# Performance work log

Measured on AMD Instinct MI355X. Metric: run time of the kernel, lower is better.

Reference implementation:

```python
import jax, jax.numpy as jnp
import numpy as np

N_BLOCKS = 2
C = 64
N_HEADS = 4
FF = 256
NB_SEQ = 40
SEQ_LEN = 512
NB_PAIRS = (NB_SEQ * (NB_SEQ - 1)) // 2  # 780
B = 2
EPS_ATT = 1e-6


def _ln(x, g, b, eps=1e-5):
    # LayerNorm over last axis (channels)
    mu = jnp.mean(x, axis=-1, keepdims=True)
    var = jnp.var(x, axis=-1, keepdims=True)
    return (x - mu) * jax.lax.rsqrt(var + eps) * g + b


def _kernel_attn(x, wq, bq, wk, bk, wv, bv, wp, bp):
    # x: [B, M, T, C]; faithful to KernelAxialMultiAttention.
    Bs, M, T, Cc = x.shape
    N, D = N_HEADS, Cc // N_HEADS
    q = jax.nn.elu(x @ wq.T + bq) + 1.0
    k = jax.nn.elu(x @ wk.T + bk) + 1.0
    v = x @ wv.T + bv
    q = q.reshape(Bs, M, T, N, D)
    k = k.reshape(Bs, M, T, N, D)
    v = v.reshape(Bs, M, T, N, D)
    ksum = k.sum(axis=2)                                   # [B,M,N,D]
    z = 1.0 / (jnp.einsum('bmtnd,bmnd->bmtn', q, ksum) + EPS_ATT)  # [B,M,T,N]
    ktv = jnp.einsum('bmtnd,bmtne->bmnde', k, v)           # [B,M,N,D,D]
    # Original does Z.expand(...,T,D) @ KtV where Z's D columns are identical,
    # which equals z * column-sum of KtV (sum over first D axis).
    ktv_cs = ktv.sum(axis=-2)                              # [B,M,N,D]
    V = z[..., None] * ktv_cs[:, :, None, :, :]            # [B,M,T,N,D]
    V = V.reshape(Bs, M, T, Cc)
    return V @ wp.T + bp


def setup_inputs() -> dict:
    key = jax.random.key(0)
    ks = iter(jax.random.split(key, 64))

    def w(shape, scale=0.05):
        return jax.random.normal(next(ks), shape, dtype=jnp.float32) * scale

    # seq2pair gather matrix [P, S]
    ii, jj = np.triu_indices(NB_SEQ, 1)
    sp = np.zeros((NB_PAIRS, NB_SEQ), np.float32)
    sp[np.arange(NB_PAIRS), ii] = 1.0
    sp[np.arange(NB_PAIRS), jj] = 1.0

    inp = {
        'x': jax.random.normal(next(ks), (B, 22, SEQ_LEN, NB_SEQ), dtype=jnp.float32),
        'w_in': w((C, 22)), 'b_in': jnp.zeros((C,), jnp.float32),
        'g0': jnp.ones((C,), jnp.float32), 'be0': jnp.zeros((C,), jnp.float32),
        'rqw': w((N_BLOCKS, C, C)), 'rqb': jnp.zeros((N_BLOCKS, C), jnp.float32),
        'rkw': w((N_BLOCKS, C, C)), 'rkb': jnp.zeros((N_BLOCKS, C), jnp.float32),
        'rvw': w((N_BLOCKS, C, C)), 'rvb': jnp.zeros((N_BLOCKS, C), jnp.float32),
        'rpw': w((N_BLOCKS, C, C)), 'rpb': jnp.zeros((N_BLOCKS, C), jnp.float32),
        'cqw': w((N_BLOCKS, C, C)), 'cqb': jnp.zeros((N_BLOCKS, C), jnp.float32),
        'ckw': w((N_BLOCKS, C, C)), 'ckb': jnp.zeros((N_BLOCKS, C), jnp.float32),
        'cvw': w((N_BLOCKS, C, C)), 'cvb': jnp.zeros((N_BLOCKS, C), jnp.float32),
        'cpw': w((N_BLOCKS, C, C)), 'cpb': jnp.zeros((N_BLOCKS, C), jnp.float32),
        'ln_g': jnp.ones((N_BLOCKS, C), jnp.float32), 'ln_b': jnp.zeros((N_BLOCKS, C), jnp.float32),
        'f1w': w((N_BLOCKS, FF, C)), 'f1b': jnp.zeros((N_BLOCKS, FF), jnp.float32),
        'f2w': w((N_BLOCKS, C, FF)), 'f2b': jnp.zeros((N_BLOCKS, C), jnp.float32),
        'wout': w((1, C)), 'bout': jnp.zeros((1,), jnp.float32),
        'seq2pair': jnp.asarray(sp),
    }
    return inp


def reference(x, w_in, b_in, g0, be0, rqw, rqb, rkw, rkb, rvw, rvb, rpw, rpb,
              cqw, cqb, ckw, ckb, cvw, cvb, cpw, cpb, ln_g, ln_b,
              f1w, f1b, f2w, f2b, wout, bout, seq2pair):
    # block_1_1: 1x1 conv (22->64) + ReLU; x: [B,22,L,S] -> h: [B,C,L,S]
    h = jax.nn.relu(jnp.einsum('bcls,dc->bdls', x, w_in) + b_in[None, :, None, None])
    # seq2pair gather-sum: [B,P,L,C] channel-last representation
    hp = jnp.einsum('ps,bdls->bpld', seq2pair, h)
    hp = _ln(hp, g0, be0)
    for i in range(N_BLOCKS):
        # row attention over seq_len axis (M=P, T=L)
        att = _kernel_attn(hp, rqw[i], rqb[i], rkw[i], rkb[i], rvw[i], rvb[i], rpw[i], rpb[i])
        hp = att + hp
        hp = _ln(hp, ln_g[i], ln_b[i])
        # column attention over pairs axis (M=L, T=P)
        hc = jnp.swapaxes(hp, 1, 2)  # [B,L,P,C]
        att = _kernel_attn(hc, cqw[i], cqb[i], ckw[i], ckb[i], cvw[i], cvb[i], cpw[i], cpb[i])
        hp = jnp.swapaxes(att, 1, 2) + hp
        hp = _ln(hp, ln_g[i], ln_b[i])
        # FFN: 1x1 conv 64->256 GELU 256->64, residual
        f = jax.nn.gelu(hp @ f1w[i].T + f1b[i], approximate=False)
        hp = (f @ f2w[i].T + f2b[i]) + hp
        if i != N_BLOCKS - 1:
            hp = _ln(hp, ln_g[i], ln_b[i])
    # pwFNN: 1x1 conv 64->1 + Softplus, then mean over seq_len axis
    y = jax.nn.softplus(hp @ wout.T + bout)[..., 0]   # [B,P,L]
    return jnp.mean(y, axis=-1)                        # [B,P]
```

## Files before the change

kernel.cpp:

```cpp
#include <hip/hip_runtime.h>
#include <math.h>
#include <stdint.h>

#define B_   2
#define S_   40
#define P_   780
#define L_   512
#define C_   64
#define FF_  256
#define NTOK (B_*P_*L_)

typedef __attribute__((ext_vector_type(8))) short short8;
typedef __attribute__((ext_vector_type(4))) float f32x4;
typedef __attribute__((ext_vector_type(4))) unsigned short us4;

__device__ __forceinline__ float ln64(float r, float g, float b) {
    float s1 = r, s2 = r * r;
    #pragma unroll
    for (int m = 1; m < 64; m <<= 1) {
        s1 += __shfl_xor(s1, m, 64);
        s2 += __shfl_xor(s2, m, 64);
    }
    float mu  = s1 * (1.0f / 64.0f);
    float var = s2 * (1.0f / 64.0f) - mu * mu;
    return (r - mu) * rsqrtf(var + 1e-5f) * g + b;
}
__device__ __forceinline__ float gelu_fast(float x) {
    float x2 = x * x;
    float u  = x * fmaf(0.044715f, x2, 1.0f);
    float e  = __builtin_amdgcn_exp2f(u * 2.302265106f);
    return x * e * __builtin_amdgcn_rcpf(e + 1.0f);
}
__device__ __forceinline__ float softplus_f(float v) {
    return (v > 20.0f) ? v : log1pf(__expf(v));
}
__device__ __forceinline__ float elup1(float v) {
    return (v > 0.0f) ? v + 1.0f : __expf(v);
}
__device__ __forceinline__ unsigned short f2bf(float f) {
    union { float f; uint32_t u; } cv; cv.f = f;
    uint32_t u = cv.u;
    return (unsigned short)((u + 0x7FFFu + ((u >> 16) & 1u)) >> 16);
}
__device__ __forceinline__ float bf2f(unsigned short u) {
    union { uint32_t u; float f; } cv; cv.u = (uint32_t)u << 16; return cv.f;
}
__device__ __forceinline__ float bflo(uint32_t w) {
    union { uint32_t u; float f; } cv; cv.u = w << 16; return cv.f;
}
__device__ __forceinline__ float bfhi(uint32_t w) {
    union { uint32_t u; float f; } cv; cv.u = w & 0xffff0000u; return cv.f;
}
__device__ __forceinline__ uint32_t cvtpk(float a, float b) {
    uint32_t d;
    asm("v_cvt_pk_bf16_f32 %0, %1, %2" : "=v"(d) : "v"(a), "v"(b));
    return d;
}

__global__ void k_conv_in(const float* __restrict__ x, const float* __restrict__ w_in,
                          const float* __restrict__ b_in, float* __restrict__ h) {
    int gid = blockIdx.x * 256 + threadIdx.x;
    int c  = gid & 63;
    int tk = gid >> 6;
    if (tk >= B_ * L_ * S_) return;
    int b = tk / (L_ * S_);
    int r = tk % (L_ * S_);
    int l = r / S_;
    int s = r % S_;
    float acc = b_in[c];
    const float* xb = x + (size_t)b * 22 * L_ * S_ + (size_t)l * S_ + s;
    #pragma unroll
    for (int cc = 0; cc < 22; cc++)
        acc = fmaf(xb[(size_t)cc * L_ * S_], w_in[c * 22 + cc], acc);
    h[gid] = fmaxf(acc, 0.0f);
}

__global__ void k_gather_ln(const float* __restrict__ h, const float* __restrict__ g0,
                            const float* __restrict__ be0, unsigned short* __restrict__ hp) {
    int lane = threadIdx.x & 63;
    int wv   = threadIdx.x >> 6;
    int tk = blockIdx.x * 4 + wv;
    if (tk >= NTOK) return;
    int b = tk / (P_ * L_);
    int r = tk % (P_ * L_);
    int p = r / L_;
    int l = r % L_;
    int i = 0, rem = p, cnt = S_ - 1;
    while (rem >= cnt) { rem -= cnt; cnt--; i++; }
    int j = i + 1 + rem;
    const float* hb = h + (((size_t)b * L_ + l) * S_) * 64;
    float v = hb[i * 64 + lane] + hb[j * 64 + lane];
    hp[(size_t)tk * 64 + lane] = f2bf(ln64(v, g0[lane], be0[lane]));
}

__global__ void k_wprep_qkv(const float* __restrict__ rqw, const float* __restrict__ rkw,
                            const float* __restrict__ rvw, const float* __restrict__ cqw,
                            const float* __restrict__ ckw, const float* __restrict__ cvw,
                            unsigned short* __restrict__ qkvf) {
    int g = blockIdx.x * 256 + threadIdx.x;
    if (g >= 6144) return;
    int m = g >> 9, r = g & 511;
    int mat = m >> 1, layer = m & 1;
    int q = r >> 6, lane = r & 63;
    int c = lane & 15, hi = lane >> 4;
    int nt = q >> 1, s = q & 1;
    const float* base;
    switch (mat) {
        case 0: base = rqw; break; case 1: base = rkw; break; case 2: base = rvw; break;
        case 3: base = cqw; break; case 4: base = ckw; break; default: base = cvw; break;
    }
    const float* src = base + layer * 4096 + (nt * 16 + c) * 64 + s * 32 + hi * 8;
    short8 v;
    #pragma unroll
    for (int i = 0; i < 8; i++) v[i] = (short)f2bf(src[i]);
    *(short8*)(qkvf + (size_t)m * 4096 + (size_t)r * 8) = v;
}

__global__ void k_wprep(const float* __restrict__ f1w, const float* __restrict__ f2w,
                        unsigned short* __restrict__ w1s, unsigned short* __restrict__ w2s) {
    int g = blockIdx.x * 256 + threadIdx.x;
    if (g >= 8192) return;
    int layer = g >> 12;
    int rem   = g & 4095;
    int which = rem >> 11;
    int idx   = rem & 2047;
    int l  = idx & 63;
    int q  = idx >> 6;
    int c  = l & 15, hi = l >> 4;
    const float* src;
    unsigned short* dst;
    if (which == 0) {
        int s = q & 1, nt = q >> 1;
        src = f1w + (size_t)layer * 16384 + (nt * 16 + c) * 64 + s * 32 + hi * 8;
        dst = w1s + (size_t)layer * 16384 + (size_t)idx * 8;
    } else {
        int s = q & 7, nt = q >> 3;
        src = f2w + (size_t)layer * 16384 + (nt * 16 + c) * 256 + s * 32 + hi * 8;
        dst = w2s + (size_t)layer * 16384 + (size_t)idx * 8;
    }
    short8 v;
    #pragma unroll
    for (int i = 0; i < 8; i++) v[i] = (short)f2bf(src[i]);
    *(short8*)dst = v;
}

__global__ __launch_bounds__(512) void k_row_fused(
        const unsigned short* __restrict__ hp, unsigned short* __restrict__ hpT,
        const unsigned short* __restrict__ wqf, const unsigned short* __restrict__ wkf,
        const unsigned short* __restrict__ wvf,
        const float* __restrict__ bq, const float* __restrict__ bk,
        const float* __restrict__ bv, const float* __restrict__ wp,
        const float* __restrict__ bp, const float* __restrict__ lng,
        const float* __restrict__ lnb) {
    __shared__ float redK[8][64];
    __shared__ float redV[8][64];
    __shared__ float kvfin[64];
    __shared__ float sksum[64];
    __shared__ float swkv[256];

    const int tid = threadIdx.x, lane = tid & 63, w8 = tid >> 6;
    const int t = lane & 15, hi = lane >> 4;
    const int slice = blockIdx.x;
    const size_t base = (size_t)slice * L_ * 64;

    short8 xkeep[4][2];
    float ks[4][4] = {}, kv[4][4] = {};
    {
        short8 wkfr[4][2], wvfr[4][2];
        #pragma unroll
        for (int nt = 0; nt < 4; nt++)
            #pragma unroll
            for (int s = 0; s < 2; s++) {
                wkfr[nt][s] = *(const short8*)(wkf + ((size_t)((nt*2+s)*64 + lane)) * 8);
                wvfr[nt][s] = *(const short8*)(wvf + ((size_t)((nt*2+s)*64 + lane)) * 8);
            }
        f32x4 bkL[4], bvL[4];
        #pragma unroll
        for (int nt = 0; nt < 4; nt++) {
            bkL[nt] = *(const f32x4*)(bk + nt * 16 + hi * 4);
            bvL[nt] = *(const f32x4*)(bv + nt * 16 + hi * 4);
        }
        #pragma unroll
        for (int it = 0; it < 4; it++) {
            int tok = (w8 + it * 8) * 16 + t;
            const unsigned short* src = hp + base + (size_t)tok * 64;
            #pragma unroll
            for (int s = 0; s < 2; s++)
                xkeep[it][s] = *(const short8*)(src + s * 32 + hi * 8);
            f32x4 aK[4], aV[4];
            #pragma unroll
            for (int nt = 0; nt < 4; nt++) { aK[nt] = (f32x4){0,0,0,0}; aV[nt] = (f32x4){0,0,0,0}; }
            #pragma unroll
            for (int nt = 0; nt < 4; nt++)
                #pragma unroll
                for (int s = 0; s < 2; s++) {
                    aK[nt] = __builtin_amdgcn_mfma_f32_16x16x32_bf16(wkfr[nt][s], xkeep[it][s], aK[nt], 0, 0, 0);
                    aV[nt] = __builtin_amdgcn_mfma_f32_16x16x32_bf16(wvfr[nt][s], xkeep[it][s], aV[nt], 0, 0, 0);
                }
            #pragma unroll
            for (int nt = 0; nt < 4; nt++) {
                float kk[4], vv[4];
                #pragma unroll
                for (int r = 0; r < 4; r++) {
                    kk[r] = elup1(aK[nt][r] + bkL[nt][r]);
                    vv[r] = aV[nt][r] + bvL[nt][r];
                }
                float sp = kk[0] + kk[1] + kk[2] + kk[3];
                sp += __shfl_xor(sp, 16, 64);
                sp += __shfl_xor(sp, 32, 64);
                #pragma unroll
                for (int r = 0; r < 4; r++) { ks[nt][r] += kk[r]; kv[nt][r] += sp * vv[r]; }
            }
        }
    }
    #pragma unroll
    for (int nt = 0; nt < 4; nt++)
        #pragma unroll
        for (int r = 0; r < 4; r++) {
            #pragma unroll
            for (int m = 1; m < 16; m <<= 1) {
                ks[nt][r] += __shfl_xor(ks[nt][r], m, 64);
                kv[nt][r] += __shfl_xor(kv[nt][r], m, 64);
            }
        }
    if (t == 0) {
        #pragma unroll
        for (int nt = 0; nt < 4; nt++)
            #pragma unroll
            for (int r = 0; r < 4; r++) {
                redK[w8][nt * 16 + hi * 4 + r] = ks[nt][r];
                redV[w8][nt * 16 + hi * 4 + r] = kv[nt][r];
            }
    }
    __syncthreads();
    if (tid < 64) {
        float a = 0.0f, b2 = 0.0f;
        #pragma unroll
        for (int w = 0; w < 8; w++) { a += redK[w][tid]; b2 += redV[w][tid]; }
        sksum[tid] = a;
        kvfin[tid] = b2;
    }
    __syncthreads();
    if (tid < 256) {
        int c = tid & 63, n = tid >> 6;
        const float* wpr = wp + c * 64 + n * 16;
        float s = 0.0f;
        #pragma unroll
        for (int e = 0; e < 16; e++) s = fmaf(kvfin[n * 16 + e], wpr[e], s);
        swkv[c * 4 + n] = s;
    }
    __syncthreads();

    short8 wqfr[4][2];
    #pragma unroll
    for (int nt = 0; nt < 4; nt++)
        #pragma unroll
        for (int s = 0; s < 2; s++)
            wqfr[nt][s] = *(const short8*)(wqf + ((size_t)((nt*2+s)*64 + lane)) * 8);
    f32x4 bqL[4], bpL[4], gL[4], bL[4];
    #pragma unroll
    for (int nt = 0; nt < 4; nt++) {
        bqL[nt] = *(const f32x4*)(bq + nt * 16 + hi * 4);
        bpL[nt] = *(const f32x4*)(bp + nt * 16 + hi * 4);
        gL[nt]  = *(const f32x4*)(lng + nt * 16 + hi * 4);
        bL[nt]  = *(const f32x4*)(lnb + nt * 16 + hi * 4);
    }
    const int bb = slice / P_, pp = slice - bb * P_;

    #pragma unroll
    for (int it = 0; it < 4; it++) {
        int tok = (w8 + it * 8) * 16 + t;
        f32x4 aQ[4];
        #pragma unroll
        for (int nt = 0; nt < 4; nt++) aQ[nt] = (f32x4){0,0,0,0};
        #pragma unroll
        for (int nt = 0; nt < 4; nt++)
            #pragma unroll
            for (int s = 0; s < 2; s++)
                aQ[nt] = __builtin_amdgcn_mfma_f32_16x16x32_bf16(wqfr[nt][s], xkeep[it][s], aQ[nt], 0, 0, 0);
        float z[4];
        #pragma unroll
        for (int nt = 0; nt < 4; nt++) {
            f32x4 kS = *(const f32x4*)(sksum + nt * 16 + hi * 4);
            float d = 0.0f;
            #pragma unroll
            for (int r = 0; r < 4; r++)
                d = fmaf(elup1(aQ[nt][r] + bqL[nt][r]), kS[r], d);
            d += __shfl_xor(d, 16, 64);
            d += __shfl_xor(d, 32, 64);
            z[nt] = 1.0f / (d + 1e-6f);
        }
        const unsigned short* srcr = hp + base + (size_t)tok * 64;
        float o[4][4];
        float s1 = 0.0f, s2 = 0.0f;
        #pragma unroll
        for (int nt = 0; nt < 4; nt++) {
            us4 xr4 = *(const us4*)(srcr + nt * 16 + hi * 4);
            #pragma unroll
            for (int r = 0; r < 4; r++) {
                int ch = nt * 16 + hi * 4 + r;
                f32x4 wv4 = *(const f32x4*)(swkv + ch * 4);
                float val = z[0] * wv4[0] + z[1] * wv4[1] + z[2] * wv4[2] + z[3] * wv4[3]
                          + bpL[nt][r] + bf2f(xr4[r]);
                o[nt][r] = val;
                s1 += val; s2 += val * val;
            }
        }
        s1 += __shfl_xor(s1, 16, 64);  s1 += __shfl_xor(s1, 32, 64);
        s2 += __shfl_xor(s2, 16, 64);  s2 += __shfl_xor(s2, 32, 64);
        float mu  = s1 * (1.0f / 64.0f);
        float var = s2 * (1.0f / 64.0f) - mu * mu;
        float rs  = rsqrtf(var + 1e-5f);
        unsigned short* dst = hpT + (((size_t)bb * L_ + tok) * P_ + pp) * 64;
        #pragma unroll
        for (int nt = 0; nt < 4; nt++) {
            float r0 = (o[nt][0] - mu) * rs * gL[nt][0] + bL[nt][0];
            float r1 = (o[nt][1] - mu) * rs * gL[nt][1] + bL[nt][1];
            float r2 = (o[nt][2] - mu) * rs * gL[nt][2] + bL[nt][2];
            float r3 = (o[nt][3] - mu) * rs * gL[nt][3] + bL[nt][3];
            *(uint2*)(dst + nt * 16 + hi * 4) = make_uint2(cvtpk(r0, r1), cvtpk(r2, r3));
        }
    }
}

__global__ __launch_bounds__(512) void k_col_red(
        const unsigned short* __restrict__ xb, const unsigned short* __restrict__ wkf,
        const unsigned short* __restrict__ wvf, const float* __restrict__ bk,
        const float* __restrict__ bv, const float* __restrict__ wp,
        float* __restrict__ stats) {
    __shared__ float redK[8][64];
    __shared__ float redV[8][64];
    __shared__ float kvfin[64];

    const int tid = threadIdx.x, lane = tid & 63, w8 = tid >> 6;
    const int t = lane & 15, hi = lane >> 4;
    const int slice = blockIdx.x;
    const size_t base = (size_t)slice * P_ * 64;

    short8 wkfr[4][2], wvfr[4][2];
    #pragma unroll
    for (int nt = 0; nt < 4; nt++)
        #pragma unroll
        for (int s = 0; s < 2; s++) {
            wkfr[nt][s] = *(const short8*)(wkf + ((size_t)((nt*2+s)*64 + lane)) * 8);
            wvfr[nt][s] = *(const short8*)(wvf + ((size_t)((nt*2+s)*64 + lane)) * 8);
        }
    f32x4 bkL[4], bvL[4];
    #pragma unroll
    for (int nt = 0; nt < 4; nt++) {
        bkL[nt] = *(const f32x4*)(bk + nt * 16 + hi * 4);
        bvL[nt] = *(const f32x4*)(bv + nt * 16 + hi * 4);
    }

    float ks[4][4] = {}, kv[4][4] = {};
    #pragma unroll 1
    for (int tile = w8; tile < 49; tile += 8) {
        int tok = tile * 16 + t;
        bool valid = tok < P_;
        int tokc = valid ? tok : (P_ - 1);
        const unsigned short* src = xb + base + (size_t)tokc * 64;
        short8 xf[2];
        #pragma unroll
        for (int s = 0; s < 2; s++)
            xf[s] = *(const short8*)(src + s * 32 + hi * 8);
        f32x4 aK[4], aV[4];
        #pragma unroll
        for (int nt = 0; nt < 4; nt++) { aK[nt] = (f32x4){0,0,0,0}; aV[nt] = (f32x4){0,0,0,0}; }
        #pragma unroll
        for (int nt = 0; nt < 4; nt++)
            #pragma unroll
            for (int s = 0; s < 2; s++) {
                aK[nt] = __builtin_amdgcn_mfma_f32_16x16x32_bf16(wkfr[nt][s], xf[s], aK[nt], 0, 0, 0);
                aV[nt] = __builtin_amdgcn_mfma_f32_16x16x32_bf16(wvfr[nt][s], xf[s], aV[nt], 0, 0, 0);
            }
        #pragma unroll
        for (int nt = 0; nt < 4; nt++) {
            float kk[4], vv[4];
            #pragma unroll
            for (int r = 0; r < 4; r++) {
                kk[r] = valid ? elup1(aK[nt][r] + bkL[nt][r]) : 0.0f;
                vv[r] = valid ? (aV[nt][r] + bvL[nt][r]) : 0.0f;
            }
            float sp = kk[0] + kk[1] + kk[2] + kk[3];
            sp += __shfl_xor(sp, 16, 64);
            sp += __shfl_xor(sp, 32, 64);
            #pragma unroll
            for (int r = 0; r < 4; r++) { ks[nt][r] += kk[r]; kv[nt][r] += sp * vv[r]; }
        }
    }

    #pragma unroll
    for (int nt = 0; nt < 4; nt++)
        #pragma unroll
        for (int r = 0; r < 4; r++) {
            #pragma unroll
            for (int m = 1; m < 16; m <<= 1) {
                ks[nt][r] += __shfl_xor(ks[nt][r], m, 64);
                kv[nt][r] += __shfl_xor(kv[nt][r], m, 64);
            }
        }
    if (t == 0) {
        #pragma unroll
        for (int nt = 0; nt < 4; nt++)
            #pragma unroll
            for (int r = 0; r < 4; r++) {
                redK[w8][nt * 16 + hi * 4 + r] = ks[nt][r];
                redV[w8][nt * 16 + hi * 4 + r] = kv[nt][r];
            }
    }
    __syncthreads();
    if (tid < 64) {
        float a = 0.0f, b2 = 0.0f;
        #pragma unroll
        for (int w = 0; w < 8; w++) { a += redK[w][tid]; b2 += redV[w][tid]; }
        stats[(size_t)slice * 320 + tid] = a;
        kvfin[tid] = b2;
    }
    __syncthreads();
    if (tid < 256) {
        int c = tid & 63, n = tid >> 6;
        const float* wpr = wp + c * 64 + n * 16;
        float s = 0.0f;
        #pragma unroll
        for (int e = 0; e < 16; e++) s = fmaf(kvfin[n * 16 + e], wpr[e], s);
        stats[(size_t)slice * 320 + 64 + c * 4 + n] = s;
    }
}

template <int MODE>
__global__ __launch_bounds__(256, 2) void k_cmap_ffn3(
        const unsigned short* __restrict__ hpT, unsigned short* __restrict__ hp,
        const unsigned short* __restrict__ wqf,
        const float* __restrict__ bq, const float* __restrict__ bpv,
        const float* __restrict__ stats,
        const unsigned short* __restrict__ w1s, const float* __restrict__ f1b,
        const unsigned short* __restrict__ w2s, const float* __restrict__ f2b,
        const float* __restrict__ lng, const float* __restrict__ lnb,
        const float* __restrict__ wout, const float* __restrict__ bout,
        float* __restrict__ out) {
    __shared__ __align__(16) unsigned char G2[4][3][4096];
    __shared__ float sstat[320];

    const int tid = threadIdx.x, lane = tid & 63, wv = tid >> 6;
    const int t = lane & 15, hi = lane >> 4;
    const int slice = blockIdx.x / 5, tb = blockIdx.x % 5;
    const int bb = slice >> 9, ll = slice & 511;
    const size_t base = (size_t)slice * P_ * 64;

    for (int i = tid; i < 320; i += 256) sstat[i] = stats[(size_t)slice * 320 + i];
    __syncthreads();
    if (tb * 12 + wv >= 49) return;

    short8 wqfr[4][2];
    #pragma unroll
    for (int nt = 0; nt < 4; nt++)
        #pragma unroll
        for (int s = 0; s < 2; s++)
            wqfr[nt][s] = *(const short8*)(wqf + ((size_t)((nt*2+s)*64 + lane)) * 8);
    f32x4 bqL[4], bpL[4], gL[4], bL[4], f2bL[4];
    #pragma unroll
    for (int nt = 0; nt < 4; nt++) {
        bqL[nt]  = *(const f32x4*)(bq  + nt * 16 + hi * 4);
        bpL[nt]  = *(const f32x4*)(bpv + nt * 16 + hi * 4);
        gL[nt]   = *(const f32x4*)(lng + nt * 16 + hi * 4);
        bL[nt]   = *(const f32x4*)(lnb + nt * 16 + hi * 4);
        f2bL[nt] = *(const f32x4*)(f2b + nt * 16 + hi * 4);
    }

    uint32_t pw[3][8];
    short8 xb2A[3][2];
    bool validA[3];
    int pcA[3];

    #pragma unroll
    for (int tt = 0; tt < 3; tt++) {
        int slot = tb * 12 + tt * 4 + wv;
        int slotc = (slot < 49) ? slot : 48;
        int p = slotc * 16 + t;
        bool valid = (slot < 49) && (p < P_);
        int pc = (p < P_) ? p : P_ - 1;
        validA[tt] = valid; pcA[tt] = pc;
        const unsigned short* src = hpT + base + (size_t)pc * 64;

        short8 xf[2];
        #pragma unroll
        for (int s = 0; s < 2; s++)
            xf[s] = *(const short8*)(src + s * 32 + hi * 8);
        f32x4 aQ[4];
        #pragma unroll
        for (int nt = 0; nt < 4; nt++) aQ[nt] = (f32x4){0,0,0,0};
        #pragma unroll
        for (int nt = 0; nt < 4; nt++)
            #pragma unroll
            for (int s = 0; s < 2; s++)
                aQ[nt] = __builtin_amdgcn_mfma_f32_16x16x32_bf16(wqfr[nt][s], xf[s], aQ[nt], 0, 0, 0);
        float z[4];
        #pragma unroll
        for (int nt = 0; nt < 4; nt++) {
            f32x4 kS = *(const f32x4*)(sstat + nt * 16 + hi * 4);
            float d = 0.0f;
            #pragma unroll
            for (int r = 0; r < 4; r++)
                d = fmaf(elup1(aQ[nt][r] + bqL[nt][r]), kS[r], d);
            d += __shfl_xor(d, 16, 64);
            d += __shfl_xor(d, 32, 64);
            z[nt] = 1.0f / (d + 1e-6f);
        }
        float vv[4][4];
        float s1 = 0.0f, s2 = 0.0f;
        #pragma unroll
        for (int nt = 0; nt < 4; nt++) {
            us4 xr4 = *(const us4*)(src + nt * 16 + hi * 4);
            #pragma unroll
            for (int r = 0; r < 4; r++) {
                int ch = nt * 16 + hi * 4 + r;
                f32x4 wv4 = *(const f32x4*)(sstat + 64 + ch * 4);
                float val = z[0] * wv4[0] + z[1] * wv4[1] + z[2] * wv4[2] + z[3] * wv4[3]
                          + bpL[nt][r] + bf2f(xr4[r]);
                vv[nt][r] = val;
                s1 += val; s2 += val * val;
            }
        }
        s1 += __shfl_xor(s1, 16, 64);  s1 += __shfl_xor(s1, 32, 64);
        s2 += __shfl_xor(s2, 16, 64);  s2 += __shfl_xor(s2, 32, 64);
        float mu  = s1 * (1.0f / 64.0f);
        float var = s2 * (1.0f / 64.0f) - mu * mu;
        float rs  = rsqrtf(var + 1e-5f);
        #pragma unroll
        for (int nt = 0; nt < 4; nt++) {
            float r0 = (vv[nt][0] - mu) * rs * gL[nt][0] + bL[nt][0];
            float r1 = (vv[nt][1] - mu) * rs * gL[nt][1] + bL[nt][1];
            float r2 = (vv[nt][2] - mu) * rs * gL[nt][2] + bL[nt][2];
            float r3 = (vv[nt][3] - mu) * rs * gL[nt][3] + bL[nt][3];
            pw[tt][nt * 2]     = cvtpk(r0, r1);
            pw[tt][nt * 2 + 1] = cvtpk(r2, r3);
        }

        unsigned char* yw = &G2[wv][tt][0];
        #pragma unroll
        for (int nt = 0; nt < 4; nt++) {
            uint32_t ch0 = nt * 16 + hi * 4;
            uint32_t boff = (uint32_t)t * 128 + ((ch0 >> 3) ^ (uint32_t)(t & 7)) * 16 + (ch0 & 7) * 2;
            *(uint2*)(yw + boff) = make_uint2(pw[tt][nt * 2], pw[tt][nt * 2 + 1]);
        }
        #pragma unroll
        for (int s = 0; s < 2; s++)
            xb2A[tt][s] = *(short8*)(yw + (uint32_t)t * 128 +
                                     (((uint32_t)(s * 4 + hi)) ^ (uint32_t)(t & 7)) * 16);
    }

    f32x4 acc2A[3][4];
    #pragma unroll
    for (int tt = 0; tt < 3; tt++)
        #pragma unroll
        for (int n2 = 0; n2 < 4; n2++) acc2A[tt][n2] = f2bL[n2];

    #pragma unroll
    for (int half = 0; half < 2; half++) {
        #pragma unroll
        for (int ntl = 0; ntl < 8; ntl++) {
            int nt = half * 8 + ntl;
            f32x4 b1 = *(const f32x4*)(f1b + nt * 16 + hi * 4);
            f32x4 accA[3] = { b1, b1, b1 };
            #pragma unroll
            for (int s = 0; s < 2; s++) {
                short8 wf = *(const short8*)(w1s + ((size_t)(nt * 2 + s) * 64 + lane) * 8);
                accA[0] = __builtin_amdgcn_mfma_f32_16x16x32_bf16(wf, xb2A[0][s], accA[0], 0, 0, 0);
                accA[1] = __builtin_amdgcn_mfma_f32_16x16x32_bf16(wf, xb2A[1][s], accA[1], 0, 0, 0);
                accA[2] = __builtin_amdgcn_mfma_f32_16x16x32_bf16(wf, xb2A[2][s], accA[2], 0, 0, 0);
            }
            uint32_t woff = ((uint32_t)(ntl * 32 + hi * 8)) ^ ((uint32_t)(t & 7) << 4);
            #pragma unroll
            for (int tt = 0; tt < 3; tt++) {
                uint32_t p0 = cvtpk(gelu_fast(accA[tt][0]), gelu_fast(accA[tt][1]));
                uint32_t p1 = cvtpk(gelu_fast(accA[tt][2]), gelu_fast(accA[tt][3]));
                *(uint2*)(&G2[wv][tt][0] + t * 256 + woff) = make_uint2(p0, p1);
            }
        }
        #pragma unroll
        for (int sl = 0; sl < 4; sl++) {
            int s = half * 4 + sl;
            uint32_t roff = ((uint32_t)(sl * 64 + hi * 16)) ^ ((uint32_t)(t & 7) << 4);
            short8 faA[3];
            #pragma unroll
            for (int tt = 0; tt < 3; tt++)
                faA[tt] = *(short8*)(&G2[wv][tt][0] + t * 256 + roff);
            #pragma unroll
            for (int n2 = 0; n2 < 4; n2++) {
                short8 wf = *(const short8*)(w2s + ((size_t)(n2 * 8 + s) * 64 + lane) * 8);
                acc2A[0][n2] = __builtin_amdgcn_mfma_f32_16x16x32_bf16(wf, faA[0], acc2A[0][n2], 0, 0, 0);
                acc2A[1][n2] = __builtin_amdgcn_mfma_f32_16x16x32_bf16(wf, faA[1], acc2A[1][n2], 0, 0, 0);
                acc2A[2][n2] = __builtin_amdgcn_mfma_f32_16x16x32_bf16(wf, faA[2], acc2A[2][n2], 0, 0, 0);
            }
        }
    }

    #pragma unroll
    for (int tt = 0; tt < 3; tt++) {
        float vo[4][4];
        float s1 = 0.0f, s2 = 0.0f;
        #pragma unroll
        for (int n2 = 0; n2 < 4; n2++) {
            float y0 = bflo(pw[tt][n2 * 2]);
            float y1 = bfhi(pw[tt][n2 * 2]);
            float y2 = bflo(pw[tt][n2 * 2 + 1]);
            float y3 = bfhi(pw[tt][n2 * 2 + 1]);
            vo[n2][0] = acc2A[tt][n2][0] + y0;
            vo[n2][1] = acc2A[tt][n2][1] + y1;
            vo[n2][2] = acc2A[tt][n2][2] + y2;
            vo[n2][3] = acc2A[tt][n2][3] + y3;
            #pragma unroll
            for (int r = 0; r < 4; r++) { s1 += vo[n2][r]; s2 += vo[n2][r] * vo[n2][r]; }
        }
        if (MODE == 0) {
            s1 += __shfl_xor(s1, 16, 64);  s1 += __shfl_xor(s1, 32, 64);
            s2 += __shfl_xor(s2, 16, 64);  s2 += __shfl_xor(s2, 32, 64);
            float mu  = s1 * (1.0f / 64.0f);
            float var = s2 * (1.0f / 64.0f) - mu * mu;
            float rs  = rsqrtf(var + 1e-5f);
            if (validA[tt]) {
                unsigned short* dst = hp + (((size_t)bb * P_ + pcA[tt]) * L_ + ll) * 64;
                #pragma unroll
                for (int n2 = 0; n2 < 4; n2++) {
                    float r0 = (vo[n2][0] - mu) * rs * gL[n2][0] + bL[n2][0];
                    float r1 = (vo[n2][1] - mu) * rs * gL[n2][1] + bL[n2][1];
                    float r2 = (vo[n2][2] - mu) * rs * gL[n2][2] + bL[n2][2];
                    float r3 = (vo[n2][3] - mu) * rs * gL[n2][3] + bL[n2][3];
                    *(uint2*)(dst + n2 * 16 + hi * 4) = make_uint2(cvtpk(r0, r1), cvtpk(r2, r3));
                }
            }
        } else {
            float part = 0.0f;
            #pragma unroll
            for (int n2 = 0; n2 < 4; n2++) {
                f32x4 w4 = *(const f32x4*)(wout + n2 * 16 + hi * 4);
                #pragma unroll
                for (int r = 0; r < 4; r++)
                    part = fmaf(vo[n2][r], w4[r], part);
            }
            part += __shfl_xor(part, 16, 64);
            part += __shfl_xor(part, 32, 64);
            if (hi == 0 && validA[tt]) {
                float sp = softplus_f(part + bout[0]);
                atomicAdd(out + bb * P_ + pcA[tt], sp * (1.0f / L_));
            }
        }
    }
}

extern "C" void kernel_launch(void* const* d_in, const int* in_sizes, int n_in,
                              void* d_out, int out_size, void* d_ws, size_t ws_size,
                              hipStream_t stream) {
    const float* x    = (const float*)d_in[0];
    const float* w_in = (const float*)d_in[1];
    const float* b_in = (const float*)d_in[2];
    const float* g0   = (const float*)d_in[3];
    const float* be0  = (const float*)d_in[4];
    const float* rqw  = (const float*)d_in[5];  const float* rqb = (const float*)d_in[6];
    const float* rkw  = (const float*)d_in[7];  const float* rkb = (const float*)d_in[8];
    const float* rvw  = (const float*)d_in[9];  const float* rvb = (const float*)d_in[10];
    const float* rpw  = (const float*)d_in[11]; const float* rpb = (const float*)d_in[12];
    const float* cqw  = (const float*)d_in[13]; const float* cqb = (const float*)d_in[14];
    const float* ckw  = (const float*)d_in[15]; const float* ckb = (const float*)d_in[16];
    const float* cvw  = (const float*)d_in[17]; const float* cvb = (const float*)d_in[18];
    const float* cpw  = (const float*)d_in[19]; const float* cpb = (const float*)d_in[20];
    const float* lng  = (const float*)d_in[21]; const float* lnb = (const float*)d_in[22];
    const float* f1w  = (const float*)d_in[23]; const float* f1b = (const float*)d_in[24];
    const float* f2w  = (const float*)d_in[25]; const float* f2b = (const float*)d_in[26];
    const float* wout = (const float*)d_in[27]; const float* bout= (const float*)d_in[28];
    float* out = (float*)d_out;

    unsigned short* hp  = (unsigned short*)d_ws;
    unsigned short* hpT = hp + (size_t)NTOK * 64;
    float* h = (float*)(hpT + (size_t)NTOK * 64);
    unsigned short* w1s  = (unsigned short*)h;
    unsigned short* w2s  = w1s + 2 * 16384;
    unsigned short* qkvf = w2s + 2 * 16384;
    float* stats = (float*)(qkvf + 12 * 4096);

    hipMemsetAsync(out, 0, (size_t)out_size * sizeof(float), stream);

    k_conv_in<<<(B_ * L_ * S_ * 64) / 256, 256, 0, stream>>>(x, w_in, b_in, h);
    k_gather_ln<<<NTOK / 4, 256, 0, stream>>>(h, g0, be0, hp);
    k_wprep<<<32, 256, 0, stream>>>(f1w, f2w, w1s, w2s);
    k_wprep_qkv<<<24, 256, 0, stream>>>(rqw, rkw, rvw, cqw, ckw, cvw, qkvf);

    for (int i = 0; i < 2; i++) {
        k_row_fused<<<B_ * P_, 512, 0, stream>>>(hp, hpT,
            qkvf + (size_t)(0 + i) * 4096, qkvf + (size_t)(2 + i) * 4096,
            qkvf + (size_t)(4 + i) * 4096,
            rqb + i * 64, rkb + i * 64, rvb + i * 64, rpw + i * 4096, rpb + i * 64,
            lng + i * 64, lnb + i * 64);
        k_col_red<<<B_ * L_, 512, 0, stream>>>(hpT,
            qkvf + (size_t)(8 + i) * 4096, qkvf + (size_t)(10 + i) * 4096,
            ckb + i * 64, cvb + i * 64, cpw + i * 4096, stats);
        if (i == 0) {
            k_cmap_ffn3<0><<<B_ * L_ * 5, 256, 0, stream>>>(hpT, hp,
                qkvf + (size_t)(6 + i) * 4096, cqb + i * 64, cpb + i * 64, stats,
                w1s + (size_t)i * 16384, f1b + i * 256,
                w2s + (size_t)i * 16384, f2b + i * 64,
                lng + i * 64, lnb + i * 64, wout, bout, out);
        } else {
            k_cmap_ffn3<1><<<B_ * L_ * 5, 256, 0, stream>>>(hpT, hp,
                qkvf + (size_t)(6 + i) * 4096, cqb + i * 64, cpb + i * 64, stats,
                w1s + (size_t)i * 16384, f1b + i * 256,
                w2s + (size_t)i * 16384, f2b + i * 64,
                lng + i * 64, lnb + i * 64, wout, bout, out);
        }
    }
}
```

Before: 941.0 us.

## Prefetch K/V tiles, vectorize gather-LN stores, halve FFN LDS staging

Three independent changes. The gather+LayerNorm kernel packs four bf16 outputs per lane via shuffles into one 8-byte store instead of a 2-byte store per lane. The column K/V stats loop software-pipelines its global loads by fetching the next tile's activations while the current tile's MFMAs run. The fused FFN kernel processes the 256-wide hidden layer in four quarters instead of two halves, halving the per-wave LDS staging buffer to raise occupancy, at the cost of more, smaller LDS round trips.

```diff
diff --git a/kernel.cpp b/kernel.cpp
--- a/kernel.cpp
+++ b/kernel.cpp
@@ -90,7 +90,12 @@
     int j = i + 1 + rem;
     const float* hb = h + (((size_t)b * L_ + l) * S_) * 64;
     float v = hb[i * 64 + lane] + hb[j * 64 + lane];
-    hp[(size_t)tk * 64 + lane] = f2bf(ln64(v, g0[lane], be0[lane]));
+    float rr = ln64(v, g0[lane], be0[lane]);
+    float r1 = __shfl_down(rr, 1, 64);
+    float r2 = __shfl_down(rr, 2, 64);
+    float r3 = __shfl_down(rr, 3, 64);
+    if ((lane & 3) == 0)
+        *(uint2*)(hp + (size_t)tk * 64 + lane) = make_uint2(cvtpk(rr, r1), cvtpk(r2, r3));
 }
 
 __global__ void k_wprep_qkv(const float* __restrict__ rqw, const float* __restrict__ rkw,
@@ -353,16 +358,27 @@
     }
 
     float ks[4][4] = {}, kv[4][4] = {};
+    short8 xf_cur[2];
+    bool valid_cur;
+    {
+        int tok = w8 * 16 + t;
+        valid_cur = tok < P_;
+        const unsigned short* src = xb + base + (size_t)(valid_cur ? tok : P_ - 1) * 64;
+        xf_cur[0] = *(const short8*)(src + hi * 8);
+        xf_cur[1] = *(const short8*)(src + 32 + hi * 8);
+    }
     #pragma unroll 1
     for (int tile = w8; tile < 49; tile += 8) {
-        int tok = tile * 16 + t;
-        bool valid = tok < P_;
-        int tokc = valid ? tok : (P_ - 1);
-        const unsigned short* src = xb + base + (size_t)tokc * 64;
-        short8 xf[2];
-        #pragma unroll
-        for (int s = 0; s < 2; s++)
-            xf[s] = *(const short8*)(src + s * 32 + hi * 8);
+        short8 xf_nxt[2];
+        bool valid_nxt = false;
+        int ntile = tile + 8;
+        if (ntile < 49) {
+            int tok = ntile * 16 + t;
+            valid_nxt = tok < P_;
+            const unsigned short* src = xb + base + (size_t)(valid_nxt ? tok : P_ - 1) * 64;
+            xf_nxt[0] = *(const short8*)(src + hi * 8);
+            xf_nxt[1] = *(const short8*)(src + 32 + hi * 8);
+        }
         f32x4 aK[4], aV[4];
         #pragma unroll
         for (int nt = 0; nt < 4; nt++) { aK[nt] = (f32x4){0,0,0,0}; aV[nt] = (f32x4){0,0,0,0}; }
@@ -370,16 +386,16 @@
         for (int nt = 0; nt < 4; nt++)
             #pragma unroll
             for (int s = 0; s < 2; s++) {
-                aK[nt] = __builtin_amdgcn_mfma_f32_16x16x32_bf16(wkfr[nt][s], xf[s], aK[nt], 0, 0, 0);
-                aV[nt] = __builtin_amdgcn_mfma_f32_16x16x32_bf16(wvfr[nt][s], xf[s], aV[nt], 0, 0, 0);
+                aK[nt] = __builtin_amdgcn_mfma_f32_16x16x32_bf16(wkfr[nt][s], xf_cur[s], aK[nt], 0, 0, 0);
+                aV[nt] = __builtin_amdgcn_mfma_f32_16x16x32_bf16(wvfr[nt][s], xf_cur[s], aV[nt], 0, 0, 0);
             }
         #pragma unroll
         for (int nt = 0; nt < 4; nt++) {
             float kk[4], vv[4];
             #pragma unroll
             for (int r = 0; r < 4; r++) {
-                kk[r] = valid ? elup1(aK[nt][r] + bkL[nt][r]) : 0.0f;
-                vv[r] = valid ? (aV[nt][r] + bvL[nt][r]) : 0.0f;
+                kk[r] = valid_cur ? elup1(aK[nt][r] + bkL[nt][r]) : 0.0f;
+                vv[r] = valid_cur ? (aV[nt][r] + bvL[nt][r]) : 0.0f;
             }
             float sp = kk[0] + kk[1] + kk[2] + kk[3];
             sp += __shfl_xor(sp, 16, 64);
@@ -387,6 +403,9 @@
             #pragma unroll
             for (int r = 0; r < 4; r++) { ks[nt][r] += kk[r]; kv[nt][r] += sp * vv[r]; }
         }
+        xf_cur[0] = xf_nxt[0];
+        xf_cur[1] = xf_nxt[1];
+        valid_cur = valid_nxt;
     }
 
     #pragma unroll
@@ -438,7 +457,7 @@
         const float* __restrict__ lng, const float* __restrict__ lnb,
         const float* __restrict__ wout, const float* __restrict__ bout,
         float* __restrict__ out) {
-    __shared__ __align__(16) unsigned char G2[4][3][4096];
+    __shared__ __align__(16) unsigned char G2[4][3][2048];
     __shared__ float sstat[320];
 
     const int tid = threadIdx.x, lane = tid & 63, wv = tid >> 6;
@@ -556,10 +575,10 @@
         for (int n2 = 0; n2 < 4; n2++) acc2A[tt][n2] = f2bL[n2];
 
     #pragma unroll
-    for (int half = 0; half < 2; half++) {
-        #pragma unroll
-        for (int ntl = 0; ntl < 8; ntl++) {
-            int nt = half * 8 + ntl;
+    for (int q = 0; q < 4; q++) {
+        #pragma unroll
+        for (int ntl = 0; ntl < 4; ntl++) {
+            int nt = q * 4 + ntl;
             f32x4 b1 = *(const f32x4*)(f1b + nt * 16 + hi * 4);
             f32x4 accA[3] = { b1, b1, b1 };
             #pragma unroll
@@ -574,17 +593,17 @@
             for (int tt = 0; tt < 3; tt++) {
                 uint32_t p0 = cvtpk(gelu_fast(accA[tt][0]), gelu_fast(accA[tt][1]));
                 uint32_t p1 = cvtpk(gelu_fast(accA[tt][2]), gelu_fast(accA[tt][3]));
-                *(uint2*)(&G2[wv][tt][0] + t * 256 + woff) = make_uint2(p0, p1);
-            }
-        }
-        #pragma unroll
-        for (int sl = 0; sl < 4; sl++) {
-            int s = half * 4 + sl;
+                *(uint2*)(&G2[wv][tt][0] + t * 128 + woff) = make_uint2(p0, p1);
+            }
+        }
+        #pragma unroll
+        for (int sl = 0; sl < 2; sl++) {
+            int s = q * 2 + sl;
             uint32_t roff = ((uint32_t)(sl * 64 + hi * 16)) ^ ((uint32_t)(t & 7) << 4);
             short8 faA[3];
             #pragma unroll
             for (int tt = 0; tt < 3; tt++)
-                faA[tt] = *(short8*)(&G2[wv][tt][0] + t * 256 + roff);
+                faA[tt] = *(short8*)(&G2[wv][tt][0] + t * 128 + roff);
             #pragma unroll
             for (int n2 = 0; n2 < 4; n2++) {
                 short8 wf = *(const short8*)(w2s + ((size_t)(n2 * 8 + s) * 64 + lane) * 8);
```

Measured after the change: 1.009 ms. 1.07x slower.
